# Kernel optimization log

Measured on AMD Instinct MI355X. Metric: run time of the kernel, lower is better.

## Reference

```python
import jax, jax.numpy as jnp
import numpy as np

B, CIN, T, H, W = 1, 256, 64, 32, 32
A, G = 8, 8
SCALES = jnp.array([1., 2., 4., 8., 16., 32., 64., 128.], dtype=jnp.float32)
FEAT_STRIDE = 8.0
NMS_TOP_N = 100
NMS_THRESH = 0.7
MIN_SIZE = 4.0
POS_THR, NEG_THR = 0.7, 0.3
NEG_INF = -1e9


def _conv3d(x, w, b, strides):
    y = jax.lax.conv_general_dilated(
        x, w, window_strides=strides, padding=[(1, 1)] * 3,
        dimension_numbers=('NCDHW', 'OIDHW', 'NCDHW'))
    return y + b[None, :, None, None, None]


def _iou(a, b):
    # 1D interval IoU; a, b broadcastable [..., 2] = (start, end)
    inter = jnp.maximum(jnp.minimum(a[..., 1], b[..., 1]) - jnp.maximum(a[..., 0], b[..., 0]), 0.0)
    union = (a[..., 1] - a[..., 0]) + (b[..., 1] - b[..., 0]) - inter
    return inter / jnp.maximum(union, 1e-6)


def _nms(boxes, scores):
    # greedy 1D NMS: boxes [N,2], scores [N] -> top NMS_TOP_N (zero-padded)
    n = scores.shape[0]
    def step(sc, _):
        i = jnp.argmax(sc)
        s, box = sc[i], boxes[i]
        sup = (_iou(box[None], boxes) > NMS_THRESH) | (jnp.arange(n) == i)
        return jnp.where(sup, NEG_INF, sc), (box, s)
    _, (kb, ks) = jax.lax.scan(step, scores, None, length=NMS_TOP_N)
    keep = ks > NEG_INF * 0.5
    return jnp.where(keep[:, None], kb, 0.0), jnp.where(keep, ks, 0.0)


def _forward(base_feat, gt_chunks, video_len, c1w, c1b, c2w, c2b, sw, sb, dw, db):
    bsz = base_feat.shape[0]
    x = _conv3d(base_feat, c1w, c1b, (1, 2, 2))
    x = _conv3d(x, c2w, c2b, (1, 2, 2))
    feat = jnp.max(x, axis=(3, 4))                       # AdaptiveMaxPool3d((None,1,1)) -> [B,512,T]
    tlen = feat.shape[2]
    score_logit = (jnp.einsum('oc,bct->bot', sw, feat) + sb[None, :, None]).reshape(bsz, 2, A, tlen)
    delta = (jnp.einsum('oc,bct->bot', dw, feat) + db[None, :, None]).reshape(bsz, 2, A, tlen)
    prob = jax.nn.softmax(score_logit, axis=1)
    logp = jax.nn.log_softmax(score_logit, axis=1)

    # anchors: A lengths x T temporal positions, flattened as a*T + t
    anchor_len = FEAT_STRIDE * SCALES                                    # [A]
    centers = (jnp.arange(tlen, dtype=jnp.float32) + 0.5) * FEAT_STRIDE  # [T]
    a_start = centers[None, :] - anchor_len[:, None] / 2                 # [A,T]
    a_end = centers[None, :] + anchor_len[:, None] / 2
    anchors = jnp.stack([a_start, a_end], -1).reshape(-1, 2)             # [N,2]
    N = A * tlen

    # ---- proposal decode + NMS ----
    dc, dl = delta[:, 0], delta[:, 1]                                    # [B,A,T]
    pc = centers[None, None, :] + dc * anchor_len[None, :, None]
    pl = anchor_len[None, :, None] * jnp.exp(jnp.clip(dl, -10.0, 10.0))
    lim = tlen * FEAT_STRIDE
    ps = jnp.clip(pc - pl / 2, 0.0, lim)
    pe = jnp.clip(pc + pl / 2, 0.0, lim)
    boxes = jnp.stack([ps, pe], -1).reshape(bsz, N, 2)
    fg = prob[:, 1].reshape(bsz, N)
    fg = jnp.where((pe - ps).reshape(bsz, N) >= MIN_SIZE, fg, NEG_INF)
    prop_coord, prop_score = jax.vmap(_nms)(boxes, fg)

    # ---- IoU-based label assignment ----
    ious = _iou(anchors[None, :, None, :], gt_chunks[:, None, :, :])     # [B,N,G]
    max_iou = ious.max(-1)
    arg = ious.argmax(-1)                                                # [B,N]
    label = jnp.where(max_iou < NEG_THR, 0, -1)
    label = jnp.where(max_iou >= POS_THR, 1, label)
    best = ious.argmax(1)                                                # best anchor per gt [B,G]
    bidx = jnp.arange(bsz)[:, None]
    label = label.at[bidx, best].set(1)
    vl = video_len.astype(jnp.float32)[:, None]
    inside = (anchors[None, :, 0] >= 0.0) & (anchors[None, :, 1] <= vl)
    label = jnp.where(inside, label, -1)

    matched = gt_chunks[bidx, arg]                                       # [B,N,2]
    gc = (matched[..., 0] + matched[..., 1]) / 2
    gl = jnp.maximum(matched[..., 1] - matched[..., 0], 1e-6)
    ac = (anchors[:, 0] + anchors[:, 1]) / 2
    al = anchors[:, 1] - anchors[:, 0]
    reg_label = jnp.stack([(gc - ac[None]) / al[None], jnp.log(gl / al[None])], -1)
    reg_label = jax.lax.stop_gradient(reg_label)                          # targets carry no grad

    # ---- losses ----
    logp2 = logp.reshape(bsz, 2, N).transpose(0, 2, 1)                   # [B,N,2]
    lab = jnp.maximum(label, 0)
    nll = -jnp.take_along_axis(logp2, lab[..., None], axis=2)[..., 0]
    mask = (label >= 0).astype(jnp.float32)
    cls_loss = (nll * mask).sum() / jnp.maximum(mask.sum(), 1.0)

    delta2 = delta.reshape(bsz, 2, N).transpose(0, 2, 1)                 # [B,N,2]
    d = delta2 - reg_label
    sl1 = jnp.where(jnp.abs(d) < 1.0, 0.5 * d * d, jnp.abs(d) - 0.5).sum(-1)
    pos = (label == 1).astype(jnp.float32)
    reg_loss = (sl1 * pos).sum() / jnp.maximum(pos.sum(), 1.0)
    return prop_coord, prop_score, cls_loss, reg_loss


def setup_inputs() -> dict:
    key = jax.random.key(0)
    ks = jax.random.split(key, 8)
    base_feat = jax.random.normal(ks[0], (B, CIN, T, H, W), jnp.float32)
    starts = jax.random.uniform(ks[1], (B, G), minval=0.0, maxval=448.0)
    lens = jax.random.uniform(ks[2], (B, G), minval=8.0, maxval=64.0)
    gt_chunks = jnp.stack([starts, jnp.clip(starts + lens, 0.0, T * FEAT_STRIDE)], -1)
    video_len = jnp.full((B,), int(T * FEAT_STRIDE), jnp.int32)
    s = 0.02
    return dict(
        base_feat=base_feat, gt_chunks=gt_chunks, video_len=video_len,
        conv1_w=jax.random.normal(ks[3], (512, CIN, 3, 3, 3), jnp.float32) * s,
        conv1_b=jnp.zeros((512,), jnp.float32),
        conv2_w=jax.random.normal(ks[4], (512, 512, 3, 3, 3), jnp.float32) * s,
        conv2_b=jnp.zeros((512,), jnp.float32),
        score_w=jax.random.normal(ks[5], (2 * A, 512), jnp.float32) * s,
        score_b=jnp.zeros((2 * A,), jnp.float32),
        delta_w=jax.random.normal(ks[6], (2 * A, 512), jnp.float32) * s,
        delta_b=jnp.zeros((2 * A,), jnp.float32),
    )


def reference(base_feat, gt_chunks, video_len, conv1_w, conv1_b, conv2_w, conv2_b, score_w, score_b, delta_w, delta_b):
    return _forward(base_feat, gt_chunks, video_len, conv1_w, conv1_b, conv2_w, conv2_b, score_w, score_b, delta_w, delta_b)
```

## Files before the change

kernel.cpp:

```cpp
#include <hip/hip_runtime.h>

typedef __attribute__((ext_vector_type(8))) _Float16 half8;
typedef __attribute__((ext_vector_type(4))) _Float16 half4;
typedef __attribute__((ext_vector_type(4))) float floatx4;

#define DI __device__ __forceinline__

DI void gl_lds16(const void* g, void* l) {
    __builtin_amdgcn_global_load_lds(
        (__attribute__((address_space(1))) void*)(g),
        (__attribute__((address_space(3))) void*)(l), 16, 0, 0);
}

__global__ void wt_split_both(const float* __restrict__ w1, _Float16* __restrict__ w1h,
                              _Float16* __restrict__ w1l, const float* __restrict__ w2,
                              _Float16* __restrict__ w2h, _Float16* __restrict__ w2l) {
    const int b = blockIdx.x;
    const float* src;
    _Float16 *dh, *dl;
    int CI;
    if (b < 512) {
        CI = 256; src = w1 + (size_t)b * CI * 27;
        dh = w1h + (size_t)b * CI * 27; dl = w1l + (size_t)b * CI * 27;
    } else {
        CI = 512; src = w2 + (size_t)(b - 512) * CI * 27;
        dh = w2h + (size_t)(b - 512) * CI * 27; dl = w2l + (size_t)(b - 512) * CI * 27;
    }
    const int K = CI * 27;
    for (int idx = threadIdx.x; idx < K; idx += blockDim.x) {
        const int ci = idx / 27;
        const int tap = idx - ci * 27;
        const float x = src[idx] * 64.0f;
        const _Float16 h = (_Float16)x;
        dh[tap * CI + ci] = h;
        dl[tap * CI + ci] = (_Float16)(x - (float)h);
    }
}

__global__ void in_split(const float* __restrict__ in, _Float16* __restrict__ oh,
                         _Float16* __restrict__ ol) {
    const int lane = threadIdx.x;
    const int ci = blockIdx.x * 64 + lane;
    const int s0 = blockIdx.y * 32;
    const float* src = in + (size_t)ci * 65536 + s0;
    float v[32];
#pragma unroll
    for (int q = 0; q < 8; ++q) *(float4*)(v + q * 4) = *(const float4*)(src + q * 4);
    const int cdst = blockIdx.x * 64 + lane;
#pragma unroll
    for (int j = 0; j < 32; ++j) {
        const _Float16 h = (_Float16)v[j];
        oh[(size_t)(s0 + j) * 256 + cdst] = h;
        ol[(size_t)(s0 + j) * 256 + cdst] = (_Float16)(v[j] - (float)h);
    }
}

__global__ __launch_bounds__(256, 2) void conv1_mfma(
        const _Float16* __restrict__ xh, const _Float16* __restrict__ xl,
        const _Float16* __restrict__ wh, const _Float16* __restrict__ wl,
        const float* __restrict__ b1,
        _Float16* __restrict__ yh, _Float16* __restrict__ yl) {
    __shared__ __align__(16) _Float16 Ah[128 * 64];
    __shared__ __align__(16) _Float16 Al[128 * 64];
    __shared__ __align__(16) _Float16 Bh[128 * 64];
    __shared__ __align__(16) _Float16 Bl[128 * 64];
    const int tid = threadIdx.x;
    const int co_blk = blockIdx.x;
    const int t = blockIdx.y;
    const int h0 = blockIdx.z * 8;
    const int wid = tid >> 6, lane = tid & 63;
    const int wm = wid & 1, wn = wid >> 1;
    const int ml = lane & 15, ql = lane >> 4;
    const int arow = lane >> 3;
    const int achk = (lane & 7) ^ arow;
    const int aslot = lane & 7;
    const int brow = tid >> 1;
    const int bsel = (tid & 1) * 4;
    const int br7 = brow & 7;
    const int bh_ = h0 + (brow >> 4), bw_ = brow & 15;
    const int cs0 = (ql ^ (ml & 7)) * 8;
    const int cs1 = ((4 + ql) ^ (ml & 7)) * 8;

    floatx4 zz = {0.f, 0.f, 0.f, 0.f};
    floatx4 acc[4][4];
#pragma unroll
    for (int i = 0; i < 4; ++i)
#pragma unroll
        for (int j = 0; j < 4; ++j) acc[i][j] = zz;

    const size_t wbo = (size_t)co_blk * 128 * 6912;

    int tap = 0, ci0 = 0;
    for (int i = 0; i < 108; ++i) {
        const int kt = tap / 9;
        const int r9 = tap - kt * 9;
        const int kh = r9 / 3;
        const int kw = r9 - kh * 3;
        const int it = t + kt - 1;
        const bool tok = ((unsigned)it < 64u);
        __syncthreads();
        {
            const size_t gb = wbo + (size_t)tap * 256 + ci0 + achk * 8;
#pragma unroll
            for (int q = 0; q < 4; ++q) {
                const int r = wid * 32 + q * 8 + arow;
                const size_t g = gb + (size_t)r * 6912;
                gl_lds16(wh + g, &Ah[r * 64 + aslot * 8]);
                gl_lds16(wl + g, &Al[r * 64 + aslot * 8]);
            }
        }
        {
            const int ih = 2 * bh_ + kh - 1, iw = 2 * bw_ + kw - 1;
            const bool ok = tok && ((unsigned)ih < 32u) && ((unsigned)iw < 32u);
            uint4 vh4[4], vl4[4];
#pragma unroll
            for (int j2 = 0; j2 < 4; ++j2) {
                vh4[j2] = make_uint4(0u, 0u, 0u, 0u);
                vl4[j2] = make_uint4(0u, 0u, 0u, 0u);
            }
            if (ok) {
                const size_t src = (((size_t)it * 32 + ih) * 32 + iw) * 256 + ci0 + bsel * 8;
#pragma unroll
                for (int j2 = 0; j2 < 4; ++j2) {
                    vh4[j2] = *(const uint4*)(xh + src + j2 * 8);
                    vl4[j2] = *(const uint4*)(xl + src + j2 * 8);
                }
            }
#pragma unroll
            for (int j2 = 0; j2 < 4; ++j2) {
                const int slot = (bsel + j2) ^ br7;
                *(uint4*)&Bh[brow * 64 + slot * 8] = vh4[j2];
                *(uint4*)&Bl[brow * 64 + slot * 8] = vl4[j2];
            }
        }
        __syncthreads();
#pragma unroll
        for (int u = 0; u < 2; ++u) {
            const int cs = (u == 0) ? cs0 : cs1;
            half8 ah[4], alo[4], bh8[4], blo[4];
#pragma unroll
            for (int mi = 0; mi < 4; ++mi) {
                ah[mi]  = *(const half8*)&Ah[(wm * 64 + mi * 16 + ml) * 64 + cs];
                alo[mi] = *(const half8*)&Al[(wm * 64 + mi * 16 + ml) * 64 + cs];
            }
#pragma unroll
            for (int ni = 0; ni < 4; ++ni) {
                bh8[ni] = *(const half8*)&Bh[(wn * 64 + ni * 16 + ml) * 64 + cs];
                blo[ni] = *(const half8*)&Bl[(wn * 64 + ni * 16 + ml) * 64 + cs];
            }
#pragma unroll
            for (int mi = 0; mi < 4; ++mi)
#pragma unroll
                for (int ni = 0; ni < 4; ++ni) {
                    acc[mi][ni] = __builtin_amdgcn_mfma_f32_16x16x32_f16(ah[mi],  bh8[ni], acc[mi][ni], 0, 0, 0);
                    acc[mi][ni] = __builtin_amdgcn_mfma_f32_16x16x32_f16(ah[mi],  blo[ni], acc[mi][ni], 0, 0, 0);
                    acc[mi][ni] = __builtin_amdgcn_mfma_f32_16x16x32_f16(alo[mi], bh8[ni], acc[mi][ni], 0, 0, 0);
                }
        }
        if (++tap == 27) { tap = 0; ci0 += 64; }
    }

    const int qr = ql * 4;
#pragma unroll
    for (int mi = 0; mi < 4; ++mi) {
        const int co = co_blk * 128 + wm * 64 + mi * 16 + qr;
#pragma unroll
        for (int ni = 0; ni < 4; ++ni) {
            const int n = wn * 64 + ni * 16 + ml;
            const int h = h0 + (n >> 4), w = n & 15;
            const size_t base = (((size_t)t * 16 + h) * 16 + w) * 512 + co;
            half4 hv, lv;
#pragma unroll
            for (int r = 0; r < 4; ++r) {
                const float v = acc[mi][ni][r] * 0.015625f + b1[co + r];
                const _Float16 hb = (_Float16)v;
                hv[r] = hb;
                lv[r] = (_Float16)(v - (float)hb);
            }
            *(half4*)(yh + base) = hv;
            *(half4*)(yl + base) = lv;
        }
    }
}

__global__ __launch_bounds__(256, 2) void conv2_mfma(
        const _Float16* __restrict__ xh, const _Float16* __restrict__ xl,
        const _Float16* __restrict__ wh, const _Float16* __restrict__ wl,
        float* __restrict__ x2p) {
    __shared__ __align__(16) _Float16 Ah[128 * 64];
    __shared__ __align__(16) _Float16 Al[128 * 64];
    __shared__ __align__(16) _Float16 Bh[128 * 64];
    __shared__ __align__(16) _Float16 Bl[128 * 64];
    const int tid = threadIdx.x;
    const int co_blk = blockIdx.x;
    const int tp = blockIdx.y;
    const int ks = blockIdx.z;
    const int wid = tid >> 6, lane = tid & 63;
    const int wm = wid & 1, wn = wid >> 1;
    const int ml = lane & 15, ql = lane >> 4;
    const int arow = lane >> 3;
    const int achk = (lane & 7) ^ arow;
    const int aslot = lane & 7;
    const int brow = tid >> 1;
    const int bsel = (tid & 1) * 4;
    const int br7 = brow & 7;
    const int btl = brow >> 6, bsp = brow & 63;
    const int bh_ = bsp >> 3, bw_ = bsp & 7;
    const int cs0 = (ql ^ (ml & 7)) * 8;
    const int cs1 = ((4 + ql) ^ (ml & 7)) * 8;

    floatx4 zz = {0.f, 0.f, 0.f, 0.f};
    floatx4 acc[4][4];
#pragma unroll
    for (int i = 0; i < 4; ++i)
#pragma unroll
        for (int j = 0; j < 4; ++j) acc[i][j] = zz;

    const size_t wbo = (size_t)co_blk * 128 * 13824;

    int tap = 0, ci0 = ks * 128;
    for (int i = 0; i < 54; ++i) {
        const int kt = tap / 9;
        const int r9 = tap - kt * 9;
        const int kh = r9 / 3;
        const int kw = r9 - kh * 3;
        __syncthreads();
        {
            const size_t gb = wbo + (size_t)tap * 512 + ci0 + achk * 8;
#pragma unroll
            for (int q = 0; q < 4; ++q) {
                const int r = wid * 32 + q * 8 + arow;
                const size_t g = gb + (size_t)r * 13824;
                gl_lds16(wh + g, &Ah[r * 64 + aslot * 8]);
                gl_lds16(wl + g, &Al[r * 64 + aslot * 8]);
            }
        }
        {
            const int it = tp * 2 + btl + kt - 1;
            const int ih = 2 * bh_ + kh - 1, iw = 2 * bw_ + kw - 1;
            const bool ok = ((unsigned)it < 64u) && ((unsigned)ih < 16u) && ((unsigned)iw < 16u);
            uint4 vh4[4], vl4[4];
#pragma unroll
            for (int j2 = 0; j2 < 4; ++j2) {
                vh4[j2] = make_uint4(0u, 0u, 0u, 0u);
                vl4[j2] = make_uint4(0u, 0u, 0u, 0u);
            }
            if (ok) {
                const size_t src = (((size_t)it * 16 + ih) * 16 + iw) * 512 + ci0 + bsel * 8;
#pragma unroll
                for (int j2 = 0; j2 < 4; ++j2) {
                    vh4[j2] = *(const uint4*)(xh + src + j2 * 8);
                    vl4[j2] = *(const uint4*)(xl + src + j2 * 8);
                }
            }
#pragma unroll
            for (int j2 = 0; j2 < 4; ++j2) {
                const int slot = (bsel + j2) ^ br7;
                *(uint4*)&Bh[brow * 64 + slot * 8] = vh4[j2];
                *(uint4*)&Bl[brow * 64 + slot * 8] = vl4[j2];
            }
        }
        __syncthreads();
#pragma unroll
        for (int u = 0; u < 2; ++u) {
            const int cs = (u == 0) ? cs0 : cs1;
            half8 ah[4], alo[4], bh8[4], blo[4];
#pragma unroll
            for (int mi = 0; mi < 4; ++mi) {
                ah[mi]  = *(const half8*)&Ah[(wm * 64 + mi * 16 + ml) * 64 + cs];
                alo[mi] = *(const half8*)&Al[(wm * 64 + mi * 16 + ml) * 64 + cs];
            }
#pragma unroll
            for (int ni = 0; ni < 4; ++ni) {
                bh8[ni] = *(const half8*)&Bh[(wn * 64 + ni * 16 + ml) * 64 + cs];
                blo[ni] = *(const half8*)&Bl[(wn * 64 + ni * 16 + ml) * 64 + cs];
            }
#pragma unroll
            for (int mi = 0; mi < 4; ++mi)
#pragma unroll
                for (int ni = 0; ni < 4; ++ni) {
                    acc[mi][ni] = __builtin_amdgcn_mfma_f32_16x16x32_f16(ah[mi],  bh8[ni], acc[mi][ni], 0, 0, 0);
                    acc[mi][ni] = __builtin_amdgcn_mfma_f32_16x16x32_f16(ah[mi],  blo[ni], acc[mi][ni], 0, 0, 0);
                    acc[mi][ni] = __builtin_amdgcn_mfma_f32_16x16x32_f16(alo[mi], bh8[ni], acc[mi][ni], 0, 0, 0);
                }
        }
        if (++tap == 27) { tap = 0; ci0 += 64; }
    }

    const int qr = ql * 4;
#pragma unroll
    for (int mi = 0; mi < 4; ++mi) {
        const int co = co_blk * 128 + wm * 64 + mi * 16 + qr;
#pragma unroll
        for (int ni = 0; ni < 4; ++ni) {
            const int n = wn * 64 + ni * 16 + ml;
            const int ng = tp * 128 + n;
            float4 v;
            v.x = acc[mi][ni][0]; v.y = acc[mi][ni][1];
            v.z = acc[mi][ni][2]; v.w = acc[mi][ni][3];
            *(float4*)&x2p[((size_t)ks * 4096 + ng) * 512 + co] = v;
        }
    }
}

__global__ void feat_reduce(const float* __restrict__ x2p,
                            const float* __restrict__ b2,
                            float* __restrict__ feat) {
    const int idx = blockIdx.x * 256 + threadIdx.x;
    const int t = idx >> 9, c = idx & 511;
    float mx = -3.4e38f;
    for (int sp = 0; sp < 64; ++sp) {
        const size_t ng = (size_t)t * 64 + sp;
        float s = x2p[ng * 512 + c]
                + x2p[((size_t)4096 + ng) * 512 + c]
                + x2p[((size_t)8192 + ng) * 512 + c]
                + x2p[((size_t)12288 + ng) * 512 + c];
        mx = fmaxf(mx, s);
    }
    feat[(size_t)t * 512 + c] = mx * 0.015625f + b2[c];
}

__global__ void head_kernel(const float* __restrict__ feat,
                            const float* __restrict__ sw,
                            const float* __restrict__ sb,
                            const float* __restrict__ dw,
                            const float* __restrict__ db,
                            float* __restrict__ scoreL,
                            float* __restrict__ deltaL) {
    __shared__ float fr[512];
    __shared__ float partial[32][8];
    const int t = blockIdx.x, tid = threadIdx.x;
    fr[tid] = feat[(size_t)t * 512 + tid];
    fr[tid + 256] = feat[(size_t)t * 512 + 256 + tid];
    __syncthreads();
    const int o = tid & 31, part = tid >> 5;
    const float* wrow = (o < 16) ? (sw + (size_t)o * 512) : (dw + (size_t)(o - 16) * 512);
    float s = 0.f;
    const int j0 = part * 64;
#pragma unroll 16
    for (int j = 0; j < 64; ++j) s += wrow[j0 + j] * fr[j0 + j];
    partial[o][part] = s;
    __syncthreads();
    if (tid < 32) {
        float tot = 0.f;
#pragma unroll
        for (int p = 0; p < 8; ++p) tot += partial[tid][p];
        tot += (tid < 16) ? sb[tid] : db[tid - 16];
        if (tid < 16) scoreL[tid * 64 + t] = tot;
        else deltaL[(tid - 16) * 64 + t] = tot;
    }
}

__global__ void nms_loss_kernel(const float* __restrict__ scoreL,
                                const float* __restrict__ deltaL,
                                const float* __restrict__ gt,
                                const int* __restrict__ video_len,
                                float* __restrict__ out) {
    const int lane = threadIdx.x & 63;
    float gsv[8], gev[8];
#pragma unroll
    for (int g = 0; g < 8; ++g) { gsv[g] = gt[2 * g]; gev[g] = gt[2 * g + 1]; }
    const float center = ((float)lane + 0.5f) * 8.0f;
    float psv[8], pev[8], fg[8], l0v[8], l1v[8], dcv[8], dlv[8];
#pragma unroll
    for (int j = 0; j < 8; ++j) {
        const float s0 = scoreL[j * 64 + lane], s1 = scoreL[(8 + j) * 64 + lane];
        const float mm = fmaxf(s0, s1);
        const float lse = mm + logf(expf(s0 - mm) + expf(s1 - mm));
        l0v[j] = s0 - lse; l1v[j] = s1 - lse;
        const float dc = deltaL[j * 64 + lane], dl = deltaL[(8 + j) * 64 + lane];
        dcv[j] = dc; dlv[j] = dl;
        const float alen = 8.0f * (float)(1 << j);
        const float pc = center + dc * alen;
        const float pl = alen * expf(fminf(fmaxf(dl, -10.0f), 10.0f));
        const float ps = fminf(fmaxf(pc - pl * 0.5f, 0.0f), 512.0f);
        const float pe = fminf(fmaxf(pc + pl * 0.5f, 0.0f), 512.0f);
        psv[j] = ps; pev[j] = pe;
        fg[j] = ((pe - ps) >= 4.0f) ? expf(l1v[j]) : -1e9f;
    }
    for (int itn = 0; itn < 100; ++itn) {
        float v = fg[0]; int idx = lane;
#pragma unroll
        for (int j = 1; j < 8; ++j) if (fg[j] > v) { v = fg[j]; idx = lane + 64 * j; }
#pragma unroll
        for (int off = 32; off > 0; off >>= 1) {
            const float ov = __shfl_down(v, off);
            const int oi = __shfl_down(idx, off);
            if (ov > v || (ov == v && oi < idx)) { v = ov; idx = oi; }
        }
        v = __shfl(v, 0); idx = __shfl(idx, 0);
        const int wj = idx >> 6, wl = idx & 63;
        float bw0 = 0.f, bw1 = 0.f;
#pragma unroll
        for (int j = 0; j < 8; ++j) if (j == wj) { bw0 = psv[j]; bw1 = pev[j]; }
        const float b0 = __shfl(bw0, wl);
        const float b1 = __shfl(bw1, wl);
        if (lane == 0) {
            const bool kept = v > -5e8f;
            out[2 * itn] = kept ? b0 : 0.0f;
            out[2 * itn + 1] = kept ? b1 : 0.0f;
            out[200 + itn] = kept ? v : 0.0f;
        }
#pragma unroll
        for (int j = 0; j < 8; ++j) {
            const int n = lane + 64 * j;
            const float inter = fmaxf(fminf(b1, pev[j]) - fmaxf(b0, psv[j]), 0.0f);
            const float uni = (b1 - b0) + (pev[j] - psv[j]) - inter;
            const float iou = inter / fmaxf(uni, 1e-6f);
            if (iou > 0.7f || n == idx) fg[j] = -1e9f;
        }
    }
    int labv[8], aggv[8];
#pragma unroll
    for (int j = 0; j < 8; ++j) {
        const float alen = 8.0f * (float)(1 << j);
        const float as_ = center - alen * 0.5f, ae_ = center + alen * 0.5f;
        float mx = -1.0f; int ag = 0;
#pragma unroll
        for (int g = 0; g < 8; ++g) {
            const float inter = fmaxf(fminf(ae_, gev[g]) - fmaxf(as_, gsv[g]), 0.0f);
            const float uni = (ae_ - as_) + (gev[g] - gsv[g]) - inter;
            const float iou = inter / fmaxf(uni, 1e-6f);
            if (iou > mx) { mx = iou; ag = g; }
        }
        labv[j] = (mx < 0.3f) ? 0 : ((mx >= 0.7f) ? 1 : -1);
        aggv[j] = ag;
    }
    for (int g = 0; g < 8; ++g) {
        float v = -1.0f; int idx = 0;
#pragma unroll
        for (int j = 0; j < 8; ++j) {
            const int n = lane + 64 * j;
            const float alen = 8.0f * (float)(1 << j);
            const float as_ = center - alen * 0.5f, ae_ = center + alen * 0.5f;
            const float inter = fmaxf(fminf(ae_, gev[g]) - fmaxf(as_, gsv[g]), 0.0f);
            const float uni = (ae_ - as_) + (gev[g] - gsv[g]) - inter;
            const float iou = inter / fmaxf(uni, 1e-6f);
            if (iou > v || (iou == v && n < idx)) { v = iou; idx = n; }
        }
#pragma unroll
        for (int off = 32; off > 0; off >>= 1) {
            const float ov = __shfl_down(v, off);
            const int oi = __shfl_down(idx, off);
            if (ov > v || (ov == v && oi < idx)) { v = ov; idx = oi; }
        }
        idx = __shfl(idx, 0);
#pragma unroll
        for (int j = 0; j < 8; ++j)
            if (lane == (idx & 63) && j == (idx >> 6)) labv[j] = 1;
    }
    const float vl = (float)video_len[0];
    float nll_s = 0.f, msk_s = 0.f, reg_s = 0.f, pos_s = 0.f;
#pragma unroll
    for (int j = 0; j < 8; ++j) {
        const float alen = 8.0f * (float)(1 << j);
        const float as_ = center - alen * 0.5f, ae_ = center + alen * 0.5f;
        int l = labv[j];
        if (!((as_ >= 0.0f) && (ae_ <= vl))) l = -1;
        if (l >= 0) {
            msk_s += 1.0f;
            nll_s -= (l == 1) ? l1v[j] : l0v[j];
            if (l == 1) {
                pos_s += 1.0f;
                float gcv = 0.f, glv = 0.f;
#pragma unroll
                for (int g = 0; g < 8; ++g)
                    if (g == aggv[j]) {
                        gcv = (gsv[g] + gev[g]) * 0.5f;
                        glv = fmaxf(gev[g] - gsv[g], 1e-6f);
                    }
                const float r0 = (gcv - center) / alen;
                const float r1 = logf(glv / alen);
                const float d0 = dcv[j] - r0, d1 = dlv[j] - r1;
                float s = (fabsf(d0) < 1.0f) ? (0.5f * d0 * d0) : (fabsf(d0) - 0.5f);
                s += (fabsf(d1) < 1.0f) ? (0.5f * d1 * d1) : (fabsf(d1) - 0.5f);
                reg_s += s;
            }
        }
    }
    float sums[4] = {nll_s, msk_s, reg_s, pos_s};
#pragma unroll
    for (int k = 0; k < 4; ++k)
#pragma unroll
        for (int off = 32; off > 0; off >>= 1) sums[k] += __shfl_down(sums[k], off);
    if (lane == 0) {
        out[300] = sums[0] / fmaxf(sums[1], 1.0f);
        out[301] = sums[2] / fmaxf(sums[3], 1.0f);
    }
}

extern "C" void kernel_launch(void* const* d_in, const int* in_sizes, int n_in,
                              void* d_out, int out_size, void* d_ws, size_t ws_size,
                              hipStream_t stream) {
    const float* base_feat = (const float*)d_in[0];
    const float* gt        = (const float*)d_in[1];
    const int*   video_len = (const int*)d_in[2];
    const float* w1        = (const float*)d_in[3];
    const float* b1        = (const float*)d_in[4];
    const float* w2        = (const float*)d_in[5];
    const float* b2        = (const float*)d_in[6];
    const float* sw        = (const float*)d_in[7];
    const float* sb        = (const float*)d_in[8];
    const float* dw        = (const float*)d_in[9];
    const float* db        = (const float*)d_in[10];

    char* ws = (char*)d_ws;
    _Float16* w1h = (_Float16*)ws;  ws += (size_t)512 * 6912 * 2;
    _Float16* w1l = (_Float16*)ws;  ws += (size_t)512 * 6912 * 2;
    _Float16* w2h = (_Float16*)ws;  ws += (size_t)512 * 13824 * 2;
    _Float16* w2l = (_Float16*)ws;  ws += (size_t)512 * 13824 * 2;
    _Float16* inh = (_Float16*)ws;  ws += (size_t)65536 * 256 * 2;
    _Float16* inl = (_Float16*)ws;  ws += (size_t)65536 * 256 * 2;
    _Float16* x1h = (_Float16*)ws;  ws += (size_t)64 * 16 * 16 * 512 * 2;
    _Float16* x1l = (_Float16*)ws;  ws += (size_t)64 * 16 * 16 * 512 * 2;
    float* feat   = (float*)ws;     ws += (size_t)64 * 512 * 4;
    float* scoreL = (float*)ws;     ws += (size_t)16 * 64 * 4;
    float* deltaL = (float*)ws;     ws += (size_t)16 * 64 * 4;
    float* x2p = (float*)inh;

    wt_split_both<<<1024, 256, 0, stream>>>(w1, w1h, w1l, w2, w2h, w2l);
    in_split<<<dim3(4, 2048), 64, 0, stream>>>(base_feat, inh, inl);
    conv1_mfma<<<dim3(4, 64, 2), 256, 0, stream>>>(inh, inl, w1h, w1l, b1, x1h, x1l);
    conv2_mfma<<<dim3(4, 32, 4), 256, 0, stream>>>(x1h, x1l, w2h, w2l, x2p);
    feat_reduce<<<128, 256, 0, stream>>>(x2p, b2, feat);
    head_kernel<<<64, 256, 0, stream>>>(feat, sw, sb, dw, db, scoreL, deltaL);
    nms_loss_kernel<<<1, 64, 0, stream>>>(scoreL, deltaL, gt, video_len,
                                          (float*)d_out);
}
```

Measured before the change: 834.1 us.

## Register-prefetch conv tiles, transpose splits via LDS, fuse feat reduce into head

Both conv kernels now load the next step's weight and activation tiles into registers while the current step's MFMAs run, then write them to LDS, replacing the direct global-to-LDS loads. The weight and input fp16 split kernels stage through shared memory so their writes become coalesced 16-byte stores instead of scattered 2-byte stores. The feature max-reduction is merged into the head kernel, which drops one launch and the intermediate feat buffer. The prefetch raises register pressure under launch bounds of 2 blocks per CU, and the fused head runs only 64 blocks for the reduction.

```diff
diff --git a/kernel.cpp b/kernel.cpp
--- a/kernel.cpp
+++ b/kernel.cpp
@@ -6,52 +6,78 @@
 
 #define DI __device__ __forceinline__
 
-DI void gl_lds16(const void* g, void* l) {
-    __builtin_amdgcn_global_load_lds(
-        (__attribute__((address_space(1))) void*)(g),
-        (__attribute__((address_space(3))) void*)(l), 16, 0, 0);
-}
-
-__global__ void wt_split_both(const float* __restrict__ w1, _Float16* __restrict__ w1h,
-                              _Float16* __restrict__ w1l, const float* __restrict__ w2,
-                              _Float16* __restrict__ w2h, _Float16* __restrict__ w2l) {
+__global__ __launch_bounds__(256) void wt_split_t(
+        const float* __restrict__ w1, _Float16* __restrict__ w1h, _Float16* __restrict__ w1l,
+        const float* __restrict__ w2, _Float16* __restrict__ w2h, _Float16* __restrict__ w2l) {
+    __shared__ float L[13824];
     const int b = blockIdx.x;
-    const float* src;
-    _Float16 *dh, *dl;
-    int CI;
+    const int tid = threadIdx.x;
     if (b < 512) {
-        CI = 256; src = w1 + (size_t)b * CI * 27;
-        dh = w1h + (size_t)b * CI * 27; dl = w1l + (size_t)b * CI * 27;
+        const float* src = w1 + (size_t)b * 6912;
+        for (int idx = tid; idx < 6912; idx += 256) L[idx] = src[idx] * 64.0f;
+        __syncthreads();
+        for (int c = tid; c < 864; c += 256) {
+            const int tap = c >> 5, ci0 = (c & 31) * 8;
+            half8 h, l;
+#pragma unroll
+            for (int j = 0; j < 8; ++j) {
+                const float x = L[(ci0 + j) * 27 + tap];
+                const _Float16 hh = (_Float16)x;
+                h[j] = hh; l[j] = (_Float16)(x - (float)hh);
+            }
+            const size_t off = (size_t)b * 6912 + tap * 256 + ci0;
+            *(half8*)&w1h[off] = h;
+            *(half8*)&w1l[off] = l;
+        }
     } else {
-        CI = 512; src = w2 + (size_t)(b - 512) * CI * 27;
-        dh = w2h + (size_t)(b - 512) * CI * 27; dl = w2l + (size_t)(b - 512) * CI * 27;
-    }
-    const int K = CI * 27;
-    for (int idx = threadIdx.x; idx < K; idx += blockDim.x) {
-        const int ci = idx / 27;
-        const int tap = idx - ci * 27;
-        const float x = src[idx] * 64.0f;
-        const _Float16 h = (_Float16)x;
-        dh[tap * CI + ci] = h;
-        dl[tap * CI + ci] = (_Float16)(x - (float)h);
-    }
-}
-
-__global__ void in_split(const float* __restrict__ in, _Float16* __restrict__ oh,
-                         _Float16* __restrict__ ol) {
-    const int lane = threadIdx.x;
-    const int ci = blockIdx.x * 64 + lane;
-    const int s0 = blockIdx.y * 32;
-    const float* src = in + (size_t)ci * 65536 + s0;
+        const float* src = w2 + (size_t)(b - 512) * 13824;
+        for (int idx = tid; idx < 13824; idx += 256) L[idx] = src[idx] * 64.0f;
+        __syncthreads();
+        for (int c = tid; c < 1728; c += 256) {
+            const int tap = c >> 6, ci0 = (c & 63) * 8;
+            half8 h, l;
+#pragma unroll
+            for (int j = 0; j < 8; ++j) {
+                const float x = L[(ci0 + j) * 27 + tap];
+                const _Float16 hh = (_Float16)x;
+                h[j] = hh; l[j] = (_Float16)(x - (float)hh);
+            }
+            const size_t off = (size_t)(b - 512) * 13824 + tap * 512 + ci0;
+            *(half8*)&w2h[off] = h;
+            *(half8*)&w2l[off] = l;
+        }
+    }
+}
+
+__global__ __launch_bounds__(256) void in_split(const float* __restrict__ in,
+                                                _Float16* __restrict__ oh,
+                                                _Float16* __restrict__ ol) {
+    __shared__ float T[128 * 65];
+    const int hb = blockIdx.x;
+    const int s0 = blockIdx.y * 64;
+    const int tid = threadIdx.x;
+    const int cil = tid >> 1, part = tid & 1;
+    const float* src = in + (size_t)(hb * 128 + cil) * 65536 + s0 + part * 32;
     float v[32];
 #pragma unroll
     for (int q = 0; q < 8; ++q) *(float4*)(v + q * 4) = *(const float4*)(src + q * 4);
-    const int cdst = blockIdx.x * 64 + lane;
-#pragma unroll
-    for (int j = 0; j < 32; ++j) {
-        const _Float16 h = (_Float16)v[j];
-        oh[(size_t)(s0 + j) * 256 + cdst] = h;
-        ol[(size_t)(s0 + j) * 256 + cdst] = (_Float16)(v[j] - (float)h);
+#pragma unroll
+    for (int j = 0; j < 32; ++j) T[cil * 65 + part * 32 + j] = v[j];
+    __syncthreads();
+#pragma unroll
+    for (int k = 0; k < 4; ++k) {
+        const int c = tid + k * 256;
+        const int sp = c >> 4, o = c & 15, ci0 = o * 8;
+        half8 h, l;
+#pragma unroll
+        for (int j = 0; j < 8; ++j) {
+            const float x = T[(ci0 + j) * 65 + sp];
+            const _Float16 hh = (_Float16)x;
+            h[j] = hh; l[j] = (_Float16)(x - (float)hh);
+        }
+        const size_t off = (size_t)(s0 + sp) * 256 + hb * 128 + ci0;
+        *(half8*)&oh[off] = h;
+        *(half8*)&ol[off] = l;
     }
 }
 
@@ -71,15 +97,21 @@
     const int wid = tid >> 6, lane = tid & 63;
     const int wm = wid & 1, wn = wid >> 1;
     const int ml = lane & 15, ql = lane >> 4;
-    const int arow = lane >> 3;
-    const int achk = (lane & 7) ^ arow;
-    const int aslot = lane & 7;
-    const int brow = tid >> 1;
-    const int bsel = (tid & 1) * 4;
-    const int br7 = brow & 7;
-    const int bh_ = h0 + (brow >> 4), bw_ = brow & 15;
     const int cs0 = (ql ^ (ml & 7)) * 8;
     const int cs1 = ((4 + ql) ^ (ml & 7)) * 8;
+    int asl[4]; size_t agof[4];
+#pragma unroll
+    for (int k = 0; k < 4; ++k) {
+        const int s = tid + k * 256;
+        const int r = s >> 3, c = s & 7;
+        asl[k] = r * 64 + (c ^ (r & 7)) * 8;
+        agof[k] = (size_t)r * 6912 + c * 8;
+    }
+    const int brow = tid >> 1, bsel = (tid & 1) * 4, br7 = brow & 7;
+    const int bh_ = h0 + (brow >> 4), bw_ = brow & 15;
+    int bslot[4];
+#pragma unroll
+    for (int j = 0; j < 4; ++j) bslot[j] = brow * 64 + ((bsel + j) ^ br7) * 8;
 
     floatx4 zz = {0.f, 0.f, 0.f, 0.f};
     floatx4 acc[4][4];
@@ -89,51 +121,50 @@
         for (int j = 0; j < 4; ++j) acc[i][j] = zz;
 
     const size_t wbo = (size_t)co_blk * 128 * 6912;
+    const uint4 z4 = make_uint4(0u, 0u, 0u, 0u);
+    uint4 rAh[4], rAl[4], rBh[4], rBl[4];
+
+    auto prefetch = [&](int tap, int ci0) {
+        const size_t ab = wbo + (size_t)tap * 256 + ci0;
+#pragma unroll
+        for (int k = 0; k < 4; ++k) {
+            rAh[k] = *(const uint4*)(wh + ab + agof[k]);
+            rAl[k] = *(const uint4*)(wl + ab + agof[k]);
+        }
+        const int kt = tap / 9, r9 = tap - kt * 9, kh = r9 / 3, kw = r9 - kh * 3;
+        const int it = t + kt - 1;
+        const int ih = 2 * bh_ + kh - 1, iw = 2 * bw_ + kw - 1;
+        const bool ok = ((unsigned)it < 64u) && ((unsigned)ih < 32u) && ((unsigned)iw < 32u);
+#pragma unroll
+        for (int j = 0; j < 4; ++j) { rBh[j] = z4; rBl[j] = z4; }
+        if (ok) {
+            const size_t src = (((size_t)it * 32 + ih) * 32 + iw) * 256 + ci0 + bsel * 8;
+#pragma unroll
+            for (int j = 0; j < 4; ++j) {
+                rBh[j] = *(const uint4*)(xh + src + j * 8);
+                rBl[j] = *(const uint4*)(xl + src + j * 8);
+            }
+        }
+    };
 
     int tap = 0, ci0 = 0;
+    prefetch(0, 0);
     for (int i = 0; i < 108; ++i) {
-        const int kt = tap / 9;
-        const int r9 = tap - kt * 9;
-        const int kh = r9 / 3;
-        const int kw = r9 - kh * 3;
-        const int it = t + kt - 1;
-        const bool tok = ((unsigned)it < 64u);
         __syncthreads();
-        {
-            const size_t gb = wbo + (size_t)tap * 256 + ci0 + achk * 8;
-#pragma unroll
-            for (int q = 0; q < 4; ++q) {
-                const int r = wid * 32 + q * 8 + arow;
-                const size_t g = gb + (size_t)r * 6912;
-                gl_lds16(wh + g, &Ah[r * 64 + aslot * 8]);
-                gl_lds16(wl + g, &Al[r * 64 + aslot * 8]);
-            }
-        }
-        {
-            const int ih = 2 * bh_ + kh - 1, iw = 2 * bw_ + kw - 1;
-            const bool ok = tok && ((unsigned)ih < 32u) && ((unsigned)iw < 32u);
-            uint4 vh4[4], vl4[4];
-#pragma unroll
-            for (int j2 = 0; j2 < 4; ++j2) {
-                vh4[j2] = make_uint4(0u, 0u, 0u, 0u);
-                vl4[j2] = make_uint4(0u, 0u, 0u, 0u);
-            }
-            if (ok) {
-                const size_t src = (((size_t)it * 32 + ih) * 32 + iw) * 256 + ci0 + bsel * 8;
-#pragma unroll
-                for (int j2 = 0; j2 < 4; ++j2) {
-                    vh4[j2] = *(const uint4*)(xh + src + j2 * 8);
-                    vl4[j2] = *(const uint4*)(xl + src + j2 * 8);
-                }
-            }
-#pragma unroll
-            for (int j2 = 0; j2 < 4; ++j2) {
-                const int slot = (bsel + j2) ^ br7;
-                *(uint4*)&Bh[brow * 64 + slot * 8] = vh4[j2];
-                *(uint4*)&Bl[brow * 64 + slot * 8] = vl4[j2];
-            }
+#pragma unroll
+        for (int k = 0; k < 4; ++k) {
+            *(uint4*)&Ah[asl[k]] = rAh[k];
+            *(uint4*)&Al[asl[k]] = rAl[k];
+        }
+#pragma unroll
+        for (int j = 0; j < 4; ++j) {
+            *(uint4*)&Bh[bslot[j]] = rBh[j];
+            *(uint4*)&Bl[bslot[j]] = rBl[j];
         }
         __syncthreads();
+        int ntap = tap + 1, nci0 = ci0;
+        if (ntap == 27) { ntap = 0; nci0 += 64; }
+        if (i + 1 < 108) prefetch(ntap, nci0);
 #pragma unroll
         for (int u = 0; u < 2; ++u) {
             const int cs = (u == 0) ? cs0 : cs1;
@@ -157,7 +188,7 @@
                     acc[mi][ni] = __builtin_amdgcn_mfma_f32_16x16x32_f16(alo[mi], bh8[ni], acc[mi][ni], 0, 0, 0);
                 }
         }
-        if (++tap == 27) { tap = 0; ci0 += 64; }
+        tap = ntap; ci0 = nci0;
     }
 
     const int qr = ql * 4;
@@ -198,16 +229,22 @@
     const int wid = tid >> 6, lane = tid & 63;
     const int wm = wid & 1, wn = wid >> 1;
     const int ml = lane & 15, ql = lane >> 4;
-    const int arow = lane >> 3;
-    const int achk = (lane & 7) ^ arow;
-    const int aslot = lane & 7;
-    const int brow = tid >> 1;
-    const int bsel = (tid & 1) * 4;
-    const int br7 = brow & 7;
+    const int cs0 = (ql ^ (ml & 7)) * 8;
+    const int cs1 = ((4 + ql) ^ (ml & 7)) * 8;
+    int asl[4]; size_t agof[4];
+#pragma unroll
+    for (int k = 0; k < 4; ++k) {
+        const int s = tid + k * 256;
+        const int r = s >> 3, c = s & 7;
+        asl[k] = r * 64 + (c ^ (r & 7)) * 8;
+        agof[k] = (size_t)r * 13824 + c * 8;
+    }
+    const int brow = tid >> 1, bsel = (tid & 1) * 4, br7 = brow & 7;
     const int btl = brow >> 6, bsp = brow & 63;
     const int bh_ = bsp >> 3, bw_ = bsp & 7;
-    const int cs0 = (ql ^ (ml & 7)) * 8;
-    const int cs1 = ((4 + ql) ^ (ml & 7)) * 8;
+    int bslot[4];
+#pragma unroll
+    for (int j = 0; j < 4; ++j) bslot[j] = brow * 64 + ((bsel + j) ^ br7) * 8;
 
     floatx4 zz = {0.f, 0.f, 0.f, 0.f};
     floatx4 acc[4][4];
@@ -217,50 +254,50 @@
         for (int j = 0; j < 4; ++j) acc[i][j] = zz;
 
     const size_t wbo = (size_t)co_blk * 128 * 13824;
+    const uint4 z4 = make_uint4(0u, 0u, 0u, 0u);
+    uint4 rAh[4], rAl[4], rBh[4], rBl[4];
+
+    auto prefetch = [&](int tap, int ci0) {
+        const size_t ab = wbo + (size_t)tap * 512 + ci0;
+#pragma unroll
+        for (int k = 0; k < 4; ++k) {
+            rAh[k] = *(const uint4*)(wh + ab + agof[k]);
+            rAl[k] = *(const uint4*)(wl + ab + agof[k]);
+        }
+        const int kt = tap / 9, r9 = tap - kt * 9, kh = r9 / 3, kw = r9 - kh * 3;
+        const int it = tp * 2 + btl + kt - 1;
+        const int ih = 2 * bh_ + kh - 1, iw = 2 * bw_ + kw - 1;
+        const bool ok = ((unsigned)it < 64u) && ((unsigned)ih < 16u) && ((unsigned)iw < 16u);
+#pragma unroll
+        for (int j = 0; j < 4; ++j) { rBh[j] = z4; rBl[j] = z4; }
+        if (ok) {
+            const size_t src = (((size_t)it * 16 + ih) * 16 + iw) * 512 + ci0 + bsel * 8;
+#pragma unroll
+            for (int j = 0; j < 4; ++j) {
+                rBh[j] = *(const uint4*)(xh + src + j * 8);
+                rBl[j] = *(const uint4*)(xl + src + j * 8);
+            }
+        }
+    };
 
     int tap = 0, ci0 = ks * 128;
+    prefetch(tap, ci0);
     for (int i = 0; i < 54; ++i) {
-        const int kt = tap / 9;
-        const int r9 = tap - kt * 9;
-        const int kh = r9 / 3;
-        const int kw = r9 - kh * 3;
         __syncthreads();
-        {
-            const size_t gb = wbo + (size_t)tap * 512 + ci0 + achk * 8;
-#pragma unroll
-            for (int q = 0; q < 4; ++q) {
-                const int r = wid * 32 + q * 8 + arow;
-                const size_t g = gb + (size_t)r * 13824;
-                gl_lds16(wh + g, &Ah[r * 64 + aslot * 8]);
-                gl_lds16(wl + g, &Al[r * 64 + aslot * 8]);
-            }
-        }
-        {
-            const int it = tp * 2 + btl + kt - 1;
-            const int ih = 2 * bh_ + kh - 1, iw = 2 * bw_ + kw - 1;
-            const bool ok = ((unsigned)it < 64u) && ((unsigned)ih < 16u) && ((unsigned)iw < 16u);
-            uint4 vh4[4], vl4[4];
-#pragma unroll
-            for (int j2 = 0; j2 < 4; ++j2) {
-                vh4[j2] = make_uint4(0u, 0u, 0u, 0u);
-                vl4[j2] = make_uint4(0u, 0u, 0u, 0u);
-            }
-            if (ok) {
-                const size_t src = (((size_t)it * 16 + ih) * 16 + iw) * 512 + ci0 + bsel * 8;
-#pragma unroll
-                for (int j2 = 0; j2 < 4; ++j2) {
-                    vh4[j2] = *(const uint4*)(xh + src + j2 * 8);
-                    vl4[j2] = *(const uint4*)(xl + src + j2 * 8);
-                }
-            }
-#pragma unroll
-            for (int j2 = 0; j2 < 4; ++j2) {
-                const int slot = (bsel + j2) ^ br7;
-                *(uint4*)&Bh[brow * 64 + slot * 8] = vh4[j2];
-                *(uint4*)&Bl[brow * 64 + slot * 8] = vl4[j2];
-            }
+#pragma unroll
+        for (int k = 0; k < 4; ++k) {
+            *(uint4*)&Ah[asl[k]] = rAh[k];
+            *(uint4*)&Al[asl[k]] = rAl[k];
+        }
+#pragma unroll
+        for (int j = 0; j < 4; ++j) {
+            *(uint4*)&Bh[bslot[j]] = rBh[j];
+            *(uint4*)&Bl[bslot[j]] = rBl[j];
         }
         __syncthreads();
+        int ntap = tap + 1, nci0 = ci0;
+        if (ntap == 27) { ntap = 0; nci0 += 64; }
+        if (i + 1 < 54) prefetch(ntap, nci0);
 #pragma unroll
         for (int u = 0; u < 2; ++u) {
             const int cs = (u == 0) ? cs0 : cs1;
@@ -284,7 +321,7 @@
                     acc[mi][ni] = __builtin_amdgcn_mfma_f32_16x16x32_f16(alo[mi], bh8[ni], acc[mi][ni], 0, 0, 0);
                 }
         }
-        if (++tap == 27) { tap = 0; ci0 += 64; }
+        tap = ntap; ci0 = nci0;
     }
 
     const int qr = ql * 4;
@@ -303,35 +340,28 @@
     }
 }
 
-__global__ void feat_reduce(const float* __restrict__ x2p,
-                            const float* __restrict__ b2,
-                            float* __restrict__ feat) {
-    const int idx = blockIdx.x * 256 + threadIdx.x;
-    const int t = idx >> 9, c = idx & 511;
-    float mx = -3.4e38f;
-    for (int sp = 0; sp < 64; ++sp) {
-        const size_t ng = (size_t)t * 64 + sp;
-        float s = x2p[ng * 512 + c]
-                + x2p[((size_t)4096 + ng) * 512 + c]
-                + x2p[((size_t)8192 + ng) * 512 + c]
-                + x2p[((size_t)12288 + ng) * 512 + c];
-        mx = fmaxf(mx, s);
-    }
-    feat[(size_t)t * 512 + c] = mx * 0.015625f + b2[c];
-}
-
-__global__ void head_kernel(const float* __restrict__ feat,
-                            const float* __restrict__ sw,
-                            const float* __restrict__ sb,
-                            const float* __restrict__ dw,
-                            const float* __restrict__ db,
-                            float* __restrict__ scoreL,
-                            float* __restrict__ deltaL) {
+__global__ __launch_bounds__(256) void feat_head(
+        const float* __restrict__ x2p, const float* __restrict__ b2,
+        const float* __restrict__ sw, const float* __restrict__ sb,
+        const float* __restrict__ dw, const float* __restrict__ db,
+        float* __restrict__ scoreL, float* __restrict__ deltaL) {
     __shared__ float fr[512];
     __shared__ float partial[32][8];
     const int t = blockIdx.x, tid = threadIdx.x;
-    fr[tid] = feat[(size_t)t * 512 + tid];
-    fr[tid + 256] = feat[(size_t)t * 512 + 256 + tid];
+#pragma unroll
+    for (int cc = 0; cc < 2; ++cc) {
+        const int c = tid + cc * 256;
+        float mx = -3.4e38f;
+        for (int sp = 0; sp < 64; ++sp) {
+            const size_t ng = (size_t)t * 64 + sp;
+            const float s = x2p[ng * 512 + c]
+                          + x2p[((size_t)4096 + ng) * 512 + c]
+                          + x2p[((size_t)8192 + ng) * 512 + c]
+                          + x2p[((size_t)12288 + ng) * 512 + c];
+            mx = fmaxf(mx, s);
+        }
+        fr[c] = mx * 0.015625f + b2[c];
+    }
     __syncthreads();
     const int o = tid & 31, part = tid >> 5;
     const float* wrow = (o < 16) ? (sw + (size_t)o * 512) : (dw + (size_t)(o - 16) * 512);
@@ -513,17 +543,15 @@
     _Float16* inl = (_Float16*)ws;  ws += (size_t)65536 * 256 * 2;
     _Float16* x1h = (_Float16*)ws;  ws += (size_t)64 * 16 * 16 * 512 * 2;
     _Float16* x1l = (_Float16*)ws;  ws += (size_t)64 * 16 * 16 * 512 * 2;
-    float* feat   = (float*)ws;     ws += (size_t)64 * 512 * 4;
     float* scoreL = (float*)ws;     ws += (size_t)16 * 64 * 4;
     float* deltaL = (float*)ws;     ws += (size_t)16 * 64 * 4;
     float* x2p = (float*)inh;
 
-    wt_split_both<<<1024, 256, 0, stream>>>(w1, w1h, w1l, w2, w2h, w2l);
-    in_split<<<dim3(4, 2048), 64, 0, stream>>>(base_feat, inh, inl);
+    wt_split_t<<<1024, 256, 0, stream>>>(w1, w1h, w1l, w2, w2h, w2l);
+    in_split<<<dim3(2, 1024), 256, 0, stream>>>(base_feat, inh, inl);
     conv1_mfma<<<dim3(4, 64, 2), 256, 0, stream>>>(inh, inl, w1h, w1l, b1, x1h, x1l);
     conv2_mfma<<<dim3(4, 32, 4), 256, 0, stream>>>(x1h, x1l, w2h, w2l, x2p);
-    feat_reduce<<<128, 256, 0, stream>>>(x2p, b2, feat);
-    head_kernel<<<64, 256, 0, stream>>>(feat, sw, sb, dw, db, scoreL, deltaL);
+    feat_head<<<64, 256, 0, stream>>>(x2p, b2, sw, sb, dw, db, scoreL, deltaL);
     nms_loss_kernel<<<1, 64, 0, stream>>>(scoreL, deltaL, gt, video_len,
                                           (float*)d_out);
 }
```

Result: slower. 1.006 ms (+20.6%).
